# Kernel tuning notes

Measured on AMD Instinct MI355X. Metric: run time of the kernel, lower is better.

Reference implementation:

```python
import jax, jax.numpy as jnp
import numpy as np

N_NODES = 100000
E_RAW = 3200000
IN_CH = 256
HID = 128
OUT = 64
N_LAYERS = 4


def setup_inputs() -> dict:
    rng = np.random.default_rng(0)
    src = rng.integers(0, N_NODES, E_RAW)
    dst = rng.integers(0, N_NODES, E_RAW)
    # drop self loops (add_self_loops appends them explicitly) and dedupe so the
    # edge list is coalesced (torch sparse .pow acts on coalesced values)
    code = src.astype(np.int64) * N_NODES + dst.astype(np.int64)
    code = np.unique(code[src != dst])
    edge_index = jnp.asarray(np.stack([code // N_NODES, code % N_NODES]), dtype=jnp.int32)

    key = jax.random.key(0)
    ks = jax.random.split(key, 6)
    stdv = 1.0 / np.sqrt(HID)
    x = jax.random.normal(ks[0], (N_NODES, IN_CH), jnp.float32)
    W_lin1 = jax.random.uniform(ks[1], (IN_CH, HID), jnp.float32, -stdv, stdv)
    b_lin1 = jnp.zeros((HID,), jnp.float32)
    W1 = jax.random.uniform(ks[2], (N_LAYERS, HID, HID), jnp.float32, -stdv, stdv)
    W2 = jax.random.uniform(ks[3], (N_LAYERS, HID, HID), jnp.float32, -stdv, stdv)
    W_lin2 = jax.random.uniform(ks[4], (HID, OUT), jnp.float32, -stdv, stdv)
    b_lin2 = jnp.zeros((OUT,), jnp.float32)
    return {"x": x, "W_lin1": W_lin1, "b_lin1": b_lin1, "W1": W1, "W2": W2,
            "W_lin2": W_lin2, "b_lin2": b_lin2, "edge_index": edge_index}


def reference(x, W_lin1, b_lin1, W1, W2, W_lin2, b_lin2, edge_index):
    n = N_NODES
    diag = jnp.arange(n, dtype=edge_index.dtype)
    # add self loops (appended last, so diagonal entries are the final n slots)
    row = jnp.concatenate([edge_index[0], diag])
    col = jnp.concatenate([edge_index[1], diag])
    deg = jax.ops.segment_sum(jnp.ones_like(row, jnp.float32), row, num_segments=n)
    inv_deg_row = 1.0 / deg[row]                     # per-edge 1/deg(src)
    a_vals = inv_deg_row                             # A_rw = D^{-1} A (incl. self loops)
    l_vals = (-inv_deg_row).at[-n:].add(1.0)         # L_rw = I - D^{-1} A (coalesced)

    def spmm(vals, X):
        return jax.ops.segment_sum(vals[:, None] * X[col], row, num_segments=n)

    h = jax.nn.relu(x @ W_lin1 + b_lin1)
    acc = jnp.zeros((n, HID), h.dtype)
    for l in range(N_LAYERS):
        o1 = h @ W1[l]
        o2 = h @ W2[l]
        if l != 0:
            # torch sparse .pow(l) = elementwise power of nonzero values
            o1 = spmm(l_vals ** l, o1)
            o2 = spmm(a_vals ** l, o2)
        if l != N_LAYERS - 1:
            o1 = spmm(a_vals, o1)
            o2 = spmm(l_vals, o2)
        acc = acc + jax.nn.relu(o1) + jax.nn.relu(o2)
    xm = acc / (2 * N_LAYERS)
    return xm @ W_lin2 + b_lin2
```

## Files before the change

kernel.cpp:

```cpp
#include <hip/hip_runtime.h>
#include <hip/hip_bf16.h>
#include <stdint.h>

#define NN   100000
#define ICH  256
#define HID  128
#define OUTF 64

typedef float  f32x4  __attribute__((ext_vector_type(4)));
typedef __bf16 bf16x8 __attribute__((ext_vector_type(8)));

__device__ __forceinline__ float bf2f(uint16_t u){
  union { uint32_t i; float f; } v; v.i = ((uint32_t)u) << 16; return v.f;
}
__device__ __forceinline__ uint16_t f2bf(float f){
  union { float f; uint32_t i; } v; v.f = f;
  uint32_t i = v.i;
  return (uint16_t)((i + 0x7FFFu + ((i >> 16) & 1u)) >> 16);
}
__device__ __forceinline__ uint32_t pack2(float a, float b){
  return (uint32_t)f2bf(a) | ((uint32_t)f2bf(b) << 16);
}

__global__ void k_csr(const int* __restrict__ row, int E, int n,
                      int* __restrict__ rp, float* __restrict__ r){
  int i = blockIdx.x * blockDim.x + threadIdx.x;
  if (i > n) return;
  int lo = 0, hi = E;
  while (lo < hi){
    int mid = (lo + hi) >> 1;
    if (row[mid] < i) lo = mid + 1; else hi = mid;
  }
  rp[i] = lo;
  if (i < n){
    int lo2 = lo, hi2 = E;
    while (lo2 < hi2){
      int mid = (lo2 + hi2) >> 1;
      if (row[mid] < i + 1) lo2 = mid + 1; else hi2 = mid;
    }
    r[i] = 1.0f / (float)(lo2 - lo + 1);
  }
}

__global__ void k_wprep(const float* __restrict__ W1, const float* __restrict__ W2,
                        const float* __restrict__ Wl1, const float* __restrict__ Wl2,
                        uint16_t* __restrict__ W1T, uint16_t* __restrict__ W2T,
                        uint16_t* __restrict__ Wl1T, uint16_t* __restrict__ Wl2T){
  int idx = blockIdx.x * blockDim.x + threadIdx.x;
  if (idx < 4 * 128 * 128){
    int l = idx >> 14, rem = idx & 16383, n = rem >> 7, k = rem & 127;
    W1T[idx] = f2bf(W1[l * 16384 + k * 128 + n]);
    W2T[idx] = f2bf(W2[l * 16384 + k * 128 + n]);
  }
  if (idx < 128 * 256){
    int n = idx >> 8, k = idx & 255;
    Wl1T[idx] = f2bf(Wl1[k * 128 + n]);
  }
  if (idx < 64 * 128){
    int n = idx >> 7, k = idx & 127;
    Wl2T[idx] = f2bf(Wl2[k * 64 + n]);
  }
}

__launch_bounds__(256)
__global__ void k_lin1m(const float* __restrict__ x, const uint16_t* __restrict__ Wl1T,
                        const float* __restrict__ b, uint16_t* __restrict__ h){
  __shared__ __align__(16) uint16_t Xs[64][264];
  const int tid = threadIdx.x;
  const int node0 = blockIdx.x * 64;
  const int wv = tid >> 6, lane = tid & 63, lr = lane & 15, lg = lane >> 4;

  #pragma unroll
  for (int i = 0; i < 16; ++i){
    int fi = tid + i * 256;
    int rrow = fi >> 6, c4 = (fi & 63) * 4;
    int nd = node0 + rrow;
    float4 f = (nd < NN) ? *(const float4*)(x + (size_t)nd * ICH + c4)
                         : make_float4(0.f, 0.f, 0.f, 0.f);
    *(uint2*)&Xs[rrow][c4] = make_uint2(pack2(f.x, f.y), pack2(f.z, f.w));
  }
  __syncthreads();

  bf16x8 bfr[2][8];
  #pragma unroll
  for (int n2 = 0; n2 < 2; ++n2){
    const int n = (2 * wv + n2) * 16 + lr;
    const uint16_t* bp = Wl1T + (size_t)n * 256 + lg * 8;
    #pragma unroll
    for (int ks = 0; ks < 8; ++ks)
      bfr[n2][ks] = __builtin_bit_cast(bf16x8, *(const uint4*)(bp + ks * 32));
  }
  float bias[2] = {b[(2 * wv + 0) * 16 + lr], b[(2 * wv + 1) * 16 + lr]};

  #pragma unroll
  for (int rt = 0; rt < 4; ++rt){
    const int row = rt * 16 + lr;
    bf16x8 af[8];
    #pragma unroll
    for (int ks = 0; ks < 8; ++ks)
      af[ks] = __builtin_bit_cast(bf16x8, *(const uint4*)&Xs[row][ks * 32 + lg * 8]);
    #pragma unroll
    for (int n2 = 0; n2 < 2; ++n2){
      f32x4 d = (f32x4){0.f, 0.f, 0.f, 0.f};
      #pragma unroll
      for (int ks = 0; ks < 8; ++ks)
        d = __builtin_amdgcn_mfma_f32_16x16x32_bf16(af[ks], bfr[n2][ks], d, 0, 0, 0);
      const int ncol = (2 * wv + n2) * 16 + lr;
      #pragma unroll
      for (int q = 0; q < 4; ++q){
        int nd = node0 + rt * 16 + lg * 4 + q;
        if (nd < NN){
          float v = d[q] + bias[n2];
          h[(size_t)nd * HID + ncol] = f2bf(v > 0.f ? v : 0.f);
        }
      }
    }
  }
}

__launch_bounds__(256)
__global__ void k_spmmA(const int* __restrict__ col, const int* __restrict__ rp,
                        const float* __restrict__ r, const uint32_t* __restrict__ h,
                        uint32_t* __restrict__ P, uint32_t* __restrict__ T1,
                        uint32_t* __restrict__ T2){
  int wid  = (blockIdx.x * blockDim.x + threadIdx.x) >> 6;
  int lane = threadIdx.x & 63;
  if (wid >= NN) return;
  int e0 = rp[wid], e1 = rp[wid + 1];
  float a0 = 0, b0 = 0, a1 = 0, b1 = 0, a2 = 0, b2 = 0;
  for (int base = e0; base < e1; base += 64){
    int tot = e1 - base;
    int cnt = tot < 64 ? tot : 64;
    int jv  = (lane < cnt) ? col[base + lane] : 0;
    int rvb = (lane < cnt) ? __builtin_bit_cast(int, r[jv]) : 0;
    int k = 0;
    for (; k + 16 <= cnt; k += 16){
      uint32_t hv[16];
      #pragma unroll
      for (int t = 0; t < 16; ++t){
        int j = __builtin_amdgcn_readlane(jv, k + t);
        hv[t] = h[((uint32_t)j << 6) + lane];
      }
      #pragma unroll
      for (int t = 0; t < 16; ++t){
        float rj = __builtin_bit_cast(float, __builtin_amdgcn_readlane(rvb, k + t));
        float r2 = rj * rj;
        float x0 = __builtin_bit_cast(float, hv[t] << 16);
        float x1 = __builtin_bit_cast(float, hv[t] & 0xFFFF0000u);
        a0 += x0;               b0 += x1;
        a1 = fmaf(rj, x0, a1);  b1 = fmaf(rj, x1, b1);
        a2 = fmaf(r2, x0, a2);  b2 = fmaf(r2, x1, b2);
      }
    }
    for (; k + 4 <= cnt; k += 4){
      uint32_t hv[4];
      #pragma unroll
      for (int t = 0; t < 4; ++t){
        int j = __builtin_amdgcn_readlane(jv, k + t);
        hv[t] = h[((uint32_t)j << 6) + lane];
      }
      #pragma unroll
      for (int t = 0; t < 4; ++t){
        float rj = __builtin_bit_cast(float, __builtin_amdgcn_readlane(rvb, k + t));
        float r2 = rj * rj;
        float x0 = __builtin_bit_cast(float, hv[t] << 16);
        float x1 = __builtin_bit_cast(float, hv[t] & 0xFFFF0000u);
        a0 += x0;               b0 += x1;
        a1 = fmaf(rj, x0, a1);  b1 = fmaf(rj, x1, b1);
        a2 = fmaf(r2, x0, a2);  b2 = fmaf(r2, x1, b2);
      }
    }
    for (; k < cnt; ++k){
      int j = __builtin_amdgcn_readlane(jv, k);
      float rj = __builtin_bit_cast(float, __builtin_amdgcn_readlane(rvb, k));
      float r2 = rj * rj;
      uint32_t hv = h[((uint32_t)j << 6) + lane];
      float x0 = __builtin_bit_cast(float, hv << 16);
      float x1 = __builtin_bit_cast(float, hv & 0xFFFF0000u);
      a0 += x0;               b0 += x1;
      a1 = fmaf(rj, x0, a1);  b1 = fmaf(rj, x1, b1);
      a2 = fmaf(r2, x0, a2);  b2 = fmaf(r2, x1, b2);
    }
  }
  size_t o = (size_t)wid * 64 + lane;
  P[o]  = pack2(a0, b0);
  T1[o] = pack2(a1, b1);
  T2[o] = pack2(a2, b2);
}

__launch_bounds__(256)
__global__ void k_spmmB(const int* __restrict__ col, const int* __restrict__ rp,
                        const float* __restrict__ r, const uint32_t* __restrict__ Pm,
                        uint32_t* __restrict__ Q1, uint32_t* __restrict__ Q2){
  int wid  = (blockIdx.x * blockDim.x + threadIdx.x) >> 6;
  int lane = threadIdx.x & 63;
  if (wid >= NN) return;
  int e0 = rp[wid], e1 = rp[wid + 1];
  float a1 = 0, b1 = 0, a2 = 0, b2 = 0;
  for (int base = e0; base < e1; base += 64){
    int tot = e1 - base;
    int cnt = tot < 64 ? tot : 64;
    int jv  = (lane < cnt) ? col[base + lane] : 0;
    int rvb = (lane < cnt) ? __builtin_bit_cast(int, r[jv]) : 0;
    int k = 0;
    for (; k + 16 <= cnt; k += 16){
      uint32_t pv[16];
      #pragma unroll
      for (int t = 0; t < 16; ++t){
        int j = __builtin_amdgcn_readlane(jv, k + t);
        pv[t] = Pm[((uint32_t)j << 6) + lane];
      }
      #pragma unroll
      for (int t = 0; t < 16; ++t){
        float rj = __builtin_bit_cast(float, __builtin_amdgcn_readlane(rvb, k + t));
        float r2 = rj * rj;
        float x0 = __builtin_bit_cast(float, pv[t] << 16);
        float x1 = __builtin_bit_cast(float, pv[t] & 0xFFFF0000u);
        a1 = fmaf(rj, x0, a1);  b1 = fmaf(rj, x1, b1);
        a2 = fmaf(r2, x0, a2);  b2 = fmaf(r2, x1, b2);
      }
    }
    for (; k + 4 <= cnt; k += 4){
      uint32_t pv[4];
      #pragma unroll
      for (int t = 0; t < 4; ++t){
        int j = __builtin_amdgcn_readlane(jv, k + t);
        pv[t] = Pm[((uint32_t)j << 6) + lane];
      }
      #pragma unroll
      for (int t = 0; t < 4; ++t){
        float rj = __builtin_bit_cast(float, __builtin_amdgcn_readlane(rvb, k + t));
        float r2 = rj * rj;
        float x0 = __builtin_bit_cast(float, pv[t] << 16);
        float x1 = __builtin_bit_cast(float, pv[t] & 0xFFFF0000u);
        a1 = fmaf(rj, x0, a1);  b1 = fmaf(rj, x1, b1);
        a2 = fmaf(r2, x0, a2);  b2 = fmaf(r2, x1, b2);
      }
    }
    for (; k < cnt; ++k){
      int j = __builtin_amdgcn_readlane(jv, k);
      float rj = __builtin_bit_cast(float, __builtin_amdgcn_readlane(rvb, k));
      float r2 = rj * rj;
      uint32_t pv = Pm[((uint32_t)j << 6) + lane];
      float x0 = __builtin_bit_cast(float, pv << 16);
      float x1 = __builtin_bit_cast(float, pv & 0xFFFF0000u);
      a1 = fmaf(rj, x0, a1);  b1 = fmaf(rj, x1, b1);
      a2 = fmaf(r2, x0, a2);  b2 = fmaf(r2, x1, b2);
    }
  }
  size_t o = (size_t)wid * 64 + lane;
  Q1[o] = pack2(a1, b1);
  Q2[o] = pack2(a2, b2);
}

__device__ __forceinline__ void ld4u(const uint32_t* p, uint32_t a[4]){
  uint4 t = *(const uint4*)p;
  a[0] = t.x; a[1] = t.y; a[2] = t.z; a[3] = t.w;
}

__launch_bounds__(256)
__global__ void k_epi2(const uint32_t* __restrict__ h,  const uint32_t* __restrict__ P,
                       const uint32_t* __restrict__ T1, const uint32_t* __restrict__ T2,
                       const uint32_t* __restrict__ Q1, const uint32_t* __restrict__ Q2,
                       const float* __restrict__ r,
                       const uint16_t* __restrict__ W1T, const uint16_t* __restrict__ W2T,
                       const uint16_t* __restrict__ Wl2T, const float* __restrict__ b2,
                       float* __restrict__ out){
  __shared__ __align__(16) uint32_t Mu[2][64][68];
  const int tid = threadIdx.x;
  const int node0 = blockIdx.x * 64;

  const int nb = tid >> 2;
  const int qc = tid & 3;
  const int nd = node0 + nb;
  const bool valid = nd < NN;
  const float rv = valid ? r[nd] : 1.f;
  const size_t ub = (size_t)nd * 64;

  const int wv   = tid >> 6;
  const int lane = tid & 63;
  const int lr   = lane & 15;
  const int lg   = lane >> 4;

  f32x4 acc[4][2];
  #pragma unroll
  for (int rt = 0; rt < 4; ++rt)
    #pragma unroll
    for (int n2 = 0; n2 < 2; ++n2)
      acc[rt][n2] = (f32x4){0.f, 0.f, 0.f, 0.f};

  #pragma unroll
  for (int l = 0; l < 4; ++l){
    __syncthreads();
    #pragma unroll
    for (int c = 0; c < 4; ++c){
      const int ui = qc * 4 + c * 16;
      uint32_t ah[4], ap[4], at1[4], at2[4], aq1[4], aq2[4];
      uint32_t o1[4], o2[4];
      if (valid){
        ld4u(h + ub + ui, ah);
        ld4u(P + ub + ui, ap);
        if (l == 1){ ld4u(Q1 + ub + ui, aq1); ld4u(T1 + ub + ui, at1); }
        if (l == 2){ ld4u(Q2 + ub + ui, aq2); ld4u(T1 + ub + ui, at1); ld4u(T2 + ub + ui, at2); }
        #pragma unroll
        for (int wq = 0; wq < 4; ++wq){
          float m1s[2], m2s[2];
          #pragma unroll
          for (int s = 0; s < 2; ++s){
            float hh = bf2f((uint16_t)(s ? (ah[wq] >> 16) : ah[wq]));
            float pp = bf2f((uint16_t)(s ? (ap[wq] >> 16) : ap[wq]));
            if (l == 0){
              float F = rv * (pp + hh);
              m1s[s] = F; m2s[s] = hh - F;
            } else if (l == 1){
              float t1 = bf2f((uint16_t)(s ? (at1[wq] >> 16) : at1[wq]));
              float q1 = bf2f((uint16_t)(s ? (aq1[wq] >> 16) : aq1[wq]));
              float F = rv * (pp + hh);
              float G = hh - F;
              m1s[s] = rv * (pp - q1 - t1 + G);
              m2s[s] = F - rv * (q1 + t1 + F);
            } else if (l == 2){
              float t1 = bf2f((uint16_t)(s ? (at1[wq] >> 16) : at1[wq]));
              float t2 = bf2f((uint16_t)(s ? (at2[wq] >> 16) : at2[wq]));
              float q2 = bf2f((uint16_t)(s ? (aq2[wq] >> 16) : aq2[wq]));
              float omr = 1.f - rv;
              float G2 = rv * rv * pp + omr * omr * hh;
              m1s[s] = rv * (q2 + pp - 2.f * t1 + t2 + G2);
              float F2 = rv * rv * (pp + hh);
              m2s[s] = F2 - rv * (q2 + t2 + F2);
            } else {
              float omr = 1.f - rv;
              float r3 = rv * rv * rv;
              m1s[s] = omr * omr * omr * hh - r3 * pp;
              m2s[s] = r3 * (pp + hh);
            }
          }
          o1[wq] = pack2(m1s[0], m1s[1]);
          o2[wq] = pack2(m2s[0], m2s[1]);
        }
      } else {
        #pragma unroll
        for (int wq = 0; wq < 4; ++wq){ o1[wq] = 0u; o2[wq] = 0u; }
      }
      *(uint4*)&Mu[0][nb][ui] = make_uint4(o1[0], o1[1], o1[2], o1[3]);
      *(uint4*)&Mu[1][nb][ui] = make_uint4(o2[0], o2[1], o2[2], o2[3]);
    }
    __syncthreads();

    #pragma unroll
    for (int m = 0; m < 2; ++m){
      const uint16_t* Wt = (m ? W2T : W1T) + (size_t)l * 128 * 128;
      bf16x8 bfr[2][4];
      #pragma unroll
      for (int n2 = 0; n2 < 2; ++n2){
        const int n = (2 * wv + n2) * 16 + lr;
        const uint16_t* bp = Wt + (size_t)n * 128 + lg * 8;
        #pragma unroll
        for (int ks = 0; ks < 4; ++ks)
          bfr[n2][ks] = __builtin_bit_cast(bf16x8, *(const uint4*)(bp + ks * 32));
      }
      #pragma unroll
      for (int rt = 0; rt < 4; ++rt){
        const int row = rt * 16 + lr;
        bf16x8 af[4];
        #pragma unroll
        for (int ks = 0; ks < 4; ++ks)
          af[ks] = __builtin_bit_cast(bf16x8, *(const uint4*)&Mu[m][row][ks * 16 + lg * 4]);
        #pragma unroll
        for (int n2 = 0; n2 < 2; ++n2){
          f32x4 d = (f32x4){0.f, 0.f, 0.f, 0.f};
          #pragma unroll
          for (int ks = 0; ks < 4; ++ks)
            d = __builtin_amdgcn_mfma_f32_16x16x32_bf16(af[ks], bfr[n2][ks], d, 0, 0, 0);
          #pragma unroll
          for (int q = 0; q < 4; ++q)
            acc[rt][n2][q] += (d[q] > 0.f ? d[q] : 0.f);
        }
      }
    }
  }

  __syncthreads();
  uint16_t* Mb = (uint16_t*)&Mu[0][0][0];
  #pragma unroll
  for (int rt = 0; rt < 4; ++rt)
    #pragma unroll
    for (int n2 = 0; n2 < 2; ++n2)
      #pragma unroll
      for (int q = 0; q < 4; ++q){
        int row = rt * 16 + lg * 4 + q;
        int colb = (2 * wv + n2) * 16 + lr;
        Mb[row * 136 + colb] = f2bf(acc[rt][n2][q] * 0.125f);
      }
  __syncthreads();

  const int arow = 16 * wv + lr;
  bf16x8 af2[4];
  #pragma unroll
  for (int ks = 0; ks < 4; ++ks)
    af2[ks] = __builtin_bit_cast(bf16x8, *(const uint4*)&Mu[0][arow][ks * 16 + lg * 4]);
  #pragma unroll
  for (int nt = 0; nt < 4; ++nt){
    f32x4 d = (f32x4){0.f, 0.f, 0.f, 0.f};
    #pragma unroll
    for (int ks = 0; ks < 4; ++ks){
      bf16x8 bfr = __builtin_bit_cast(bf16x8,
          *(const uint4*)(Wl2T + (size_t)(nt * 16 + lr) * 128 + ks * 32 + lg * 8));
      d = __builtin_amdgcn_mfma_f32_16x16x32_bf16(af2[ks], bfr, d, 0, 0, 0);
    }
    float bias = b2[nt * 16 + lr];
    #pragma unroll
    for (int q = 0; q < 4; ++q){
      int rr = node0 + 16 * wv + lg * 4 + q;
      if (rr < NN) out[(size_t)rr * OUTF + nt * 16 + lr] = d[q] + bias;
    }
  }
}

extern "C" void kernel_launch(void* const* d_in, const int* in_sizes, int n_in,
                              void* d_out, int out_size, void* d_ws, size_t ws_size,
                              hipStream_t stream){
  const float* x   = (const float*)d_in[0];
  const float* Wl1 = (const float*)d_in[1];
  const float* bl1 = (const float*)d_in[2];
  const float* W1  = (const float*)d_in[3];
  const float* W2  = (const float*)d_in[4];
  const float* Wl2 = (const float*)d_in[5];
  const float* bl2 = (const float*)d_in[6];
  const int*   ei  = (const int*)d_in[7];
  int E = in_sizes[7] / 2;
  const int* rowp = ei;
  const int* colp = ei + E;

  char* ws = (char*)d_ws;
  size_t off = 0;
  auto alloc = [&](size_t bytes) -> void* {
    void* p = ws + off;
    off += (bytes + 255) & ~(size_t)255;
    return p;
  };
  const size_t MATB = (size_t)NN * HID * 2;
  uint32_t* h  = (uint32_t*)alloc(MATB);
  uint32_t* P  = (uint32_t*)alloc(MATB);
  uint32_t* T1 = (uint32_t*)alloc(MATB);
  uint32_t* T2 = (uint32_t*)alloc(MATB);
  uint32_t* Q1 = (uint32_t*)alloc(MATB);
  uint32_t* Q2 = (uint32_t*)alloc(MATB);
  float* r  = (float*)alloc((size_t)NN * 4);
  int* rp   = (int*)alloc((size_t)(NN + 1) * 4);
  uint16_t* W1T  = (uint16_t*)alloc((size_t)4 * 128 * 128 * 2);
  uint16_t* W2T  = (uint16_t*)alloc((size_t)4 * 128 * 128 * 2);
  uint16_t* Wl1T = (uint16_t*)alloc((size_t)128 * 256 * 2);
  uint16_t* Wl2T = (uint16_t*)alloc((size_t)64 * 128 * 2);

  k_wprep<<<(4 * 128 * 128 + 255) / 256, 256, 0, stream>>>(W1, W2, Wl1, Wl2,
                                                           W1T, W2T, Wl1T, Wl2T);
  k_csr<<<(NN + 1 + 255) / 256, 256, 0, stream>>>(rowp, E, NN, rp, r);
  k_lin1m<<<(NN + 63) / 64, 256, 0, stream>>>(x, Wl1T, bl1, (uint16_t*)h);
  k_spmmA<<<(NN + 3) / 4, 256, 0, stream>>>(colp, rp, r, h, P, T1, T2);
  k_spmmB<<<(NN + 3) / 4, 256, 0, stream>>>(colp, rp, r, P, Q1, Q2);
  k_epi2<<<(NN + 63) / 64, 256, 0, stream>>>(h, P, T1, T2, Q1, Q2, r,
                                             W1T, W2T, Wl2T, bl2, (float*)d_out);
}
```

Baseline: 447.3 us.

## Build MFMA A-fragments directly in registers, dropping LDS staging in epilogue

The epilogue kernel now has each wave own 16 node rows and build its MFMA A-operand fragments straight from global loads in registers. This removes the per-layer shared-memory round trip and both __syncthreads barriers. Each wave now covers all 8 output column tiles, so it reads the full weight matrix from global/L2 instead of a quarter of it. Out-of-range rows are clamped to the last node rather than zeroed.

```diff
diff --git a/kernel.cpp b/kernel.cpp
--- a/kernel.cpp
+++ b/kernel.cpp
@@ -259,146 +259,116 @@
 }
 
 __launch_bounds__(256)
-__global__ void k_epi2(const uint32_t* __restrict__ h,  const uint32_t* __restrict__ P,
+__global__ void k_epi3(const uint32_t* __restrict__ h,  const uint32_t* __restrict__ P,
                        const uint32_t* __restrict__ T1, const uint32_t* __restrict__ T2,
                        const uint32_t* __restrict__ Q1, const uint32_t* __restrict__ Q2,
                        const float* __restrict__ r,
                        const uint16_t* __restrict__ W1T, const uint16_t* __restrict__ W2T,
                        const uint16_t* __restrict__ Wl2T, const float* __restrict__ b2,
                        float* __restrict__ out){
-  __shared__ __align__(16) uint32_t Mu[2][64][68];
+  __shared__ __align__(16) uint32_t Mu[64][68];
   const int tid = threadIdx.x;
   const int node0 = blockIdx.x * 64;
-
-  const int nb = tid >> 2;
-  const int qc = tid & 3;
-  const int nd = node0 + nb;
-  const bool valid = nd < NN;
-  const float rv = valid ? r[nd] : 1.f;
-  const size_t ub = (size_t)nd * 64;
-
-  const int wv   = tid >> 6;
-  const int lane = tid & 63;
-  const int lr   = lane & 15;
-  const int lg   = lane >> 4;
-
-  f32x4 acc[4][2];
-  #pragma unroll
-  for (int rt = 0; rt < 4; ++rt)
-    #pragma unroll
-    for (int n2 = 0; n2 < 2; ++n2)
-      acc[rt][n2] = (f32x4){0.f, 0.f, 0.f, 0.f};
+  const int wv = tid >> 6, lane = tid & 63, lr = lane & 15, lg = lane >> 4;
+
+  const int rowA = node0 + wv * 16 + lr;
+  const int rn = rowA < NN ? rowA : NN - 1;
+  const float rv = r[rn];
+  const size_t ub = (size_t)rn * 64;
+
+  f32x4 acc[8];
+  #pragma unroll
+  for (int nt = 0; nt < 8; ++nt) acc[nt] = (f32x4){0.f, 0.f, 0.f, 0.f};
 
   #pragma unroll
   for (int l = 0; l < 4; ++l){
-    __syncthreads();
-    #pragma unroll
-    for (int c = 0; c < 4; ++c){
-      const int ui = qc * 4 + c * 16;
+    uint4 m1f[4], m2f[4];
+    #pragma unroll
+    for (int ks = 0; ks < 4; ++ks){
+      const int uo = ks * 16 + lg * 4;
       uint32_t ah[4], ap[4], at1[4], at2[4], aq1[4], aq2[4];
+      ld4u(h + ub + uo, ah);
+      ld4u(P + ub + uo, ap);
+      if (l == 1){ ld4u(Q1 + ub + uo, aq1); ld4u(T1 + ub + uo, at1); }
+      if (l == 2){ ld4u(Q2 + ub + uo, aq2); ld4u(T1 + ub + uo, at1); ld4u(T2 + ub + uo, at2); }
       uint32_t o1[4], o2[4];
-      if (valid){
-        ld4u(h + ub + ui, ah);
-        ld4u(P + ub + ui, ap);
-        if (l == 1){ ld4u(Q1 + ub + ui, aq1); ld4u(T1 + ub + ui, at1); }
-        if (l == 2){ ld4u(Q2 + ub + ui, aq2); ld4u(T1 + ub + ui, at1); ld4u(T2 + ub + ui, at2); }
+      #pragma unroll
+      for (int w = 0; w < 4; ++w){
+        float m1s[2], m2s[2];
         #pragma unroll
-        for (int wq = 0; wq < 4; ++wq){
-          float m1s[2], m2s[2];
-          #pragma unroll
-          for (int s = 0; s < 2; ++s){
-            float hh = bf2f((uint16_t)(s ? (ah[wq] >> 16) : ah[wq]));
-            float pp = bf2f((uint16_t)(s ? (ap[wq] >> 16) : ap[wq]));
-            if (l == 0){
-              float F = rv * (pp + hh);
-              m1s[s] = F; m2s[s] = hh - F;
-            } else if (l == 1){
-              float t1 = bf2f((uint16_t)(s ? (at1[wq] >> 16) : at1[wq]));
-              float q1 = bf2f((uint16_t)(s ? (aq1[wq] >> 16) : aq1[wq]));
-              float F = rv * (pp + hh);
-              float G = hh - F;
-              m1s[s] = rv * (pp - q1 - t1 + G);
-              m2s[s] = F - rv * (q1 + t1 + F);
-            } else if (l == 2){
-              float t1 = bf2f((uint16_t)(s ? (at1[wq] >> 16) : at1[wq]));
-              float t2 = bf2f((uint16_t)(s ? (at2[wq] >> 16) : at2[wq]));
-              float q2 = bf2f((uint16_t)(s ? (aq2[wq] >> 16) : aq2[wq]));
-              float omr = 1.f - rv;
-              float G2 = rv * rv * pp + omr * omr * hh;
-              m1s[s] = rv * (q2 + pp - 2.f * t1 + t2 + G2);
-              float F2 = rv * rv * (pp + hh);
-              m2s[s] = F2 - rv * (q2 + t2 + F2);
-            } else {
-              float omr = 1.f - rv;
-              float r3 = rv * rv * rv;
-              m1s[s] = omr * omr * omr * hh - r3 * pp;
-              m2s[s] = r3 * (pp + hh);
-            }
+        for (int s = 0; s < 2; ++s){
+          float hh = bf2f((uint16_t)(s ? (ah[w] >> 16) : ah[w]));
+          float pp = bf2f((uint16_t)(s ? (ap[w] >> 16) : ap[w]));
+          if (l == 0){
+            float F = rv * (pp + hh);
+            m1s[s] = F; m2s[s] = hh - F;
+          } else if (l == 1){
+            float t1 = bf2f((uint16_t)(s ? (at1[w] >> 16) : at1[w]));
+            float q1 = bf2f((uint16_t)(s ? (aq1[w] >> 16) : aq1[w]));
+            float F = rv * (pp + hh);
+            float G = hh - F;
+            m1s[s] = rv * (pp - q1 - t1 + G);
+            m2s[s] = F - rv * (q1 + t1 + F);
+          } else if (l == 2){
+            float t1 = bf2f((uint16_t)(s ? (at1[w] >> 16) : at1[w]));
+            float t2 = bf2f((uint16_t)(s ? (at2[w] >> 16) : at2[w]));
+            float q2 = bf2f((uint16_t)(s ? (aq2[w] >> 16) : aq2[w]));
+            float omr = 1.f - rv;
+            float G2 = rv * rv * pp + omr * omr * hh;
+            m1s[s] = rv * (q2 + pp - 2.f * t1 + t2 + G2);
+            float F2 = rv * rv * (pp + hh);
+            m2s[s] = F2 - rv * (q2 + t2 + F2);
+          } else {
+            float omr = 1.f - rv;
+            float r3 = rv * rv * rv;
+            m1s[s] = omr * omr * omr * hh - r3 * pp;
+            m2s[s] = r3 * (pp + hh);
           }
-          o1[wq] = pack2(m1s[0], m1s[1]);
-          o2[wq] = pack2(m2s[0], m2s[1]);
         }
-      } else {
-        #pragma unroll
-        for (int wq = 0; wq < 4; ++wq){ o1[wq] = 0u; o2[wq] = 0u; }
-      }
-      *(uint4*)&Mu[0][nb][ui] = make_uint4(o1[0], o1[1], o1[2], o1[3]);
-      *(uint4*)&Mu[1][nb][ui] = make_uint4(o2[0], o2[1], o2[2], o2[3]);
-    }
-    __syncthreads();
+        o1[w] = pack2(m1s[0], m1s[1]);
+        o2[w] = pack2(m2s[0], m2s[1]);
+      }
+      m1f[ks] = make_uint4(o1[0], o1[1], o1[2], o1[3]);
+      m2f[ks] = make_uint4(o2[0], o2[1], o2[2], o2[3]);
+    }
 
     #pragma unroll
     for (int m = 0; m < 2; ++m){
       const uint16_t* Wt = (m ? W2T : W1T) + (size_t)l * 128 * 128;
-      bf16x8 bfr[2][4];
-      #pragma unroll
-      for (int n2 = 0; n2 < 2; ++n2){
-        const int n = (2 * wv + n2) * 16 + lr;
-        const uint16_t* bp = Wt + (size_t)n * 128 + lg * 8;
+      const uint4* mf = m ? m2f : m1f;
+      #pragma unroll
+      for (int nt = 0; nt < 8; ++nt){
+        const uint16_t* bp = Wt + (size_t)(nt * 16 + lr) * 128 + lg * 8;
+        f32x4 d = (f32x4){0.f, 0.f, 0.f, 0.f};
         #pragma unroll
-        for (int ks = 0; ks < 4; ++ks)
-          bfr[n2][ks] = __builtin_bit_cast(bf16x8, *(const uint4*)(bp + ks * 32));
-      }
-      #pragma unroll
-      for (int rt = 0; rt < 4; ++rt){
-        const int row = rt * 16 + lr;
-        bf16x8 af[4];
+        for (int ks = 0; ks < 4; ++ks){
+          bf16x8 bfr = __builtin_bit_cast(bf16x8, *(const uint4*)(bp + ks * 32));
+          d = __builtin_amdgcn_mfma_f32_16x16x32_bf16(
+                __builtin_bit_cast(bf16x8, mf[ks]), bfr, d, 0, 0, 0);
+        }
         #pragma unroll
-        for (int ks = 0; ks < 4; ++ks)
-          af[ks] = __builtin_bit_cast(bf16x8, *(const uint4*)&Mu[m][row][ks * 16 + lg * 4]);
-        #pragma unroll
-        for (int n2 = 0; n2 < 2; ++n2){
-          f32x4 d = (f32x4){0.f, 0.f, 0.f, 0.f};
-          #pragma unroll
-          for (int ks = 0; ks < 4; ++ks)
-            d = __builtin_amdgcn_mfma_f32_16x16x32_bf16(af[ks], bfr[n2][ks], d, 0, 0, 0);
-          #pragma unroll
-          for (int q = 0; q < 4; ++q)
-            acc[rt][n2][q] += (d[q] > 0.f ? d[q] : 0.f);
-        }
-      }
-    }
-  }
-
-  __syncthreads();
-  uint16_t* Mb = (uint16_t*)&Mu[0][0][0];
-  #pragma unroll
-  for (int rt = 0; rt < 4; ++rt)
-    #pragma unroll
-    for (int n2 = 0; n2 < 2; ++n2)
-      #pragma unroll
-      for (int q = 0; q < 4; ++q){
-        int row = rt * 16 + lg * 4 + q;
-        int colb = (2 * wv + n2) * 16 + lr;
-        Mb[row * 136 + colb] = f2bf(acc[rt][n2][q] * 0.125f);
-      }
+        for (int q = 0; q < 4; ++q)
+          acc[nt][q] += (d[q] > 0.f ? d[q] : 0.f);
+      }
+    }
+  }
+
+  uint16_t* Mb = (uint16_t*)&Mu[0][0];
+  #pragma unroll
+  for (int nt = 0; nt < 8; ++nt)
+    #pragma unroll
+    for (int q = 0; q < 4; ++q){
+      int row = wv * 16 + lg * 4 + q;
+      int colb = nt * 16 + lr;
+      Mb[row * 136 + colb] = f2bf(acc[nt][q] * 0.125f);
+    }
   __syncthreads();
 
   const int arow = 16 * wv + lr;
   bf16x8 af2[4];
   #pragma unroll
   for (int ks = 0; ks < 4; ++ks)
-    af2[ks] = __builtin_bit_cast(bf16x8, *(const uint4*)&Mu[0][arow][ks * 16 + lg * 4]);
+    af2[ks] = __builtin_bit_cast(bf16x8, *(const uint4*)&Mu[arow][ks * 16 + lg * 4]);
   #pragma unroll
   for (int nt = 0; nt < 4; ++nt){
     f32x4 d = (f32x4){0.f, 0.f, 0.f, 0.f};
@@ -459,6 +429,6 @@
   k_lin1m<<<(NN + 63) / 64, 256, 0, stream>>>(x, Wl1T, bl1, (uint16_t*)h);
   k_spmmA<<<(NN + 3) / 4, 256, 0, stream>>>(colp, rp, r, h, P, T1, T2);
   k_spmmB<<<(NN + 3) / 4, 256, 0, stream>>>(colp, rp, r, P, Q1, Q2);
-  k_epi2<<<(NN + 63) / 64, 256, 0, stream>>>(h, P, T1, T2, Q1, Q2, r,
+  k_epi3<<<(NN + 63) / 64, 256, 0, stream>>>(h, P, T1, T2, Q1, Q2, r,
                                              W1T, W2T, Wl2T, bl2, (float*)d_out);
 }
```

Result: slower. 547.3 us (+22.4%).
